# Optimization experiments

Measured on AMD Instinct MI355X. Metric: run time of the kernel, lower is better.

The kernel has to match this reference:

```python
import jax, jax.numpy as jnp
import numpy as np

B = 16
N = [20000, 5000, 1250, 313, 79]          # node counts per pooling level (fine -> coarse)
E = [120000, 30000, 7500, 1878, 474]      # ~6 edges per node (triangle mesh)
FILTERS = [3, 32, 32, 64, 64, 64]
K = 6
Z = 64
COND = 2
N_LAYERS = 4


def setup_inputs():
    ks = iter(jax.random.split(jax.random.key(0), 64))
    inp = {}
    inp["x"] = jax.random.normal(next(ks), (B * N[0], FILTERS[0]), jnp.float32)
    inp["label"] = jax.random.normal(next(ks), (B, COND), jnp.float32)
    for i in range(5):
        inp[f"edges{i}"] = jax.random.randint(next(ks), (2, E[i]), 0, N[i])
    for i in range(4):
        inp[f"ds_idx{i}"] = jax.random.randint(next(ks), (N[i + 1],), 0, N[i])
        inp[f"us_idx{i}"] = jax.random.randint(next(ks), (N[i], 3), 0, N[i + 1])
        inp[f"us_w{i}"] = jax.random.uniform(next(ks), (N[i], 3), jnp.float32)
    for i in range(4):
        inp[f"enc_w{i}"] = 0.1 * jax.random.normal(next(ks), (K, FILTERS[i], FILTERS[i + 1]), jnp.float32)
        inp[f"enc_b{i}"] = 0.1 * jax.random.normal(next(ks), (FILTERS[i + 1],), jnp.float32)
    for i in range(5):
        inp[f"dec_w{i}"] = 0.1 * jax.random.normal(next(ks), (K, FILTERS[-i - 1], FILTERS[-i - 2]), jnp.float32)
    for i in range(4):
        inp[f"dec_b{i}"] = 0.1 * jax.random.normal(next(ks), (FILTERS[-i - 2],), jnp.float32)
    lat_in = N[4] * FILTERS[-1]
    inp["enc_mu_w"] = 0.1 * jax.random.normal(next(ks), (lat_in, Z), jnp.float32)
    inp["enc_mu_b"] = jnp.zeros((Z,), jnp.float32)
    inp["enc_lv_w"] = 0.1 * jax.random.normal(next(ks), (lat_in, Z), jnp.float32)
    inp["enc_lv_b"] = jnp.zeros((Z,), jnp.float32)
    inp["dec_lin_w"] = 0.1 * jax.random.normal(next(ks), (Z + COND, lat_in), jnp.float32)
    inp["dec_lin_b"] = jnp.zeros((lat_in,), jnp.float32)
    return inp


def _sym_norm(edges, n):
    # ChebConv_Coma.norm: norm = D^-1/2[row] * w * D^-1/2[col], unit weights
    row, col = edges[0], edges[1]
    deg = jnp.zeros((n,), jnp.float32).at[row].add(1.0)
    dinv = jnp.where(deg > 0, deg ** -0.5, 0.0)
    return dinv[row] * dinv[col]


def _cheb(x, edges, norm, W, b):
    # Chebyshev recursion: Tx_0=x, Tx_1=L~x, Tx_k=2 L~ Tx_{k-1} - Tx_{k-2}
    src, tgt = edges[0], edges[1]

    def prop(h):  # h: [B, Nn, F] -> scatter-sum of norm-weighted source features
        return jnp.zeros_like(h).at[:, tgt].add(h[:, src] * norm[None, :, None])

    Tx0 = x
    out = jnp.einsum('bnf,fg->bng', Tx0, W[0])
    Tx1 = prop(x)
    out = out + jnp.einsum('bnf,fg->bng', Tx1, W[1])
    for k in range(2, W.shape[0]):
        Tx2 = 2.0 * prop(Tx1) - Tx0
        out = out + jnp.einsum('bnf,fg->bng', Tx2, W[k])
        Tx0, Tx1 = Tx1, Tx2
    return out if b is None else out + b


def _forward(x, label, us_ws, enc_ws, enc_bs, dec_ws, dec_bs,
             enc_mu_w, enc_mu_b, enc_lv_w, enc_lv_b, dec_lin_w, dec_lin_b,
             edges, norms, ds_idx, us_idx):
    h = x.reshape(B, N[0], FILTERS[0])
    # encoder
    for i in range(N_LAYERS):
        h = jax.nn.relu(_cheb(h, edges[i], norms[i], enc_ws[i], enc_bs[i]))
        h = h[:, ds_idx[i]]  # binary downsample matrix == row gather
    h = h.reshape(B, N[4] * FILTERS[-1])
    mu = h @ enc_mu_w + enc_mu_b
    logvar = h @ enc_lv_w + enc_lv_b
    # reparameterize (fixed eps for determinism)
    eps = jax.random.normal(jax.random.key(42), mu.shape, mu.dtype)
    z = mu + eps * jnp.exp(0.5 * logvar)
    # decoder
    h = jnp.concatenate([z, label], axis=1)
    h = jax.nn.relu(h @ dec_lin_w + dec_lin_b).reshape(B, N[4], FILTERS[-1])
    for i in range(N_LAYERS):
        lvl = N_LAYERS - 1 - i
        # barycentric upsample: 3 nonzeros per output row
        h = jnp.einsum('rk,brkf->brf', us_ws[lvl], h[:, us_idx[lvl]])
        h = jax.nn.relu(_cheb(h, edges[lvl], norms[lvl], dec_ws[i], dec_bs[i]))
    # faithful quirk of the original: final conv uses A_edge_index[-1] (coarsest graph edges)
    h = _cheb(h, edges[-1], norms[-1], dec_ws[4], None)
    return h.reshape(-1, FILTERS[0]), mu, logvar


def reference(x, label,
              edges0, edges1, edges2, edges3, edges4,
              ds_idx0, ds_idx1, ds_idx2, ds_idx3,
              us_idx0, us_idx1, us_idx2, us_idx3,
              us_w0, us_w1, us_w2, us_w3,
              enc_w0, enc_w1, enc_w2, enc_w3,
              enc_b0, enc_b1, enc_b2, enc_b3,
              dec_w0, dec_w1, dec_w2, dec_w3, dec_w4,
              dec_b0, dec_b1, dec_b2, dec_b3,
              enc_mu_w, enc_mu_b, enc_lv_w, enc_lv_b, dec_lin_w, dec_lin_b):
    edges = [edges0, edges1, edges2, edges3, edges4]
    norms = [_sym_norm(edges[i], N[i]) for i in range(5)]
    return _forward(x, label,
                    [us_w0, us_w1, us_w2, us_w3],
                    [enc_w0, enc_w1, enc_w2, enc_w3],
                    [enc_b0, enc_b1, enc_b2, enc_b3],
                    [dec_w0, dec_w1, dec_w2, dec_w3, dec_w4],
                    [dec_b0, dec_b1, dec_b2, dec_b3],
                    enc_mu_w, enc_mu_b, enc_lv_w, enc_lv_b, dec_lin_w, dec_lin_b,
                    edges, norms,
                    [ds_idx0, ds_idx1, ds_idx2, ds_idx3],
                    [us_idx0, us_idx1, us_idx2, us_idx3])
```

## Files before the change

kernel.cpp:

```cpp
#include <hip/hip_runtime.h>
#include <cstdint>
#include <cstddef>

#define WG 256
#define NB 16


struct IP5 { const int* e[5]; };
struct Ptr3 { const float* p[3]; };
struct WComb { const float* w[8]; float* c[8]; };

static __device__ __forceinline__ void fma4(float4& a, float s, const float4& b) {
  a.x = fmaf(s, b.x, a.x); a.y = fmaf(s, b.y, a.y);
  a.z = fmaf(s, b.z, a.z); a.w = fmaf(s, b.w, a.w);
}


__global__ void k_zero_i(int* __restrict__ p, int n) {
  int i = blockIdx.x * WG + threadIdx.x;
  if (i < n) p[i] = 0;
}

__global__ void k_hist_all(IP5 ep, int* __restrict__ dsrc, int* __restrict__ dtgt) {
  int i = blockIdx.x * WG + threadIdx.x;
  if (i >= 159852) return;
  int l, eo, ee, no, co;
  if (i < 120000)      { l = 0; eo = 0;      ee = 120000; no = 0;     co = 0; }
  else if (i < 150000) { l = 1; eo = 120000; ee = 30000;  no = 20000; co = 20000; }
  else if (i < 157500) { l = 2; eo = 150000; ee = 7500;   no = 25000; co = 25000; }
  else if (i < 159378) { l = 3; eo = 157500; ee = 1878;   no = 26250; co = 26250; }
  else                 { l = 4; eo = 159378; ee = 474;    no = 26563; co = 26563; }
  int e = i - eo;
  const int* E = ep.e[l];
  atomicAdd(&dsrc[no + E[e]], 1);
  atomicAdd(&dtgt[co + E[ee + e]], 1);
}

__global__ void k_scan_all(const int* __restrict__ deg_all, int* __restrict__ rowptr_all,
                           int* __restrict__ cursor_all) {
  static const int Ns[5] = {20000, 5000, 1250, 313, 20000};
  static const int CO[5] = {0, 20000, 25000, 26250, 26563};
  static const int RO[5] = {0, 20001, 25002, 26253, 26567};
  __shared__ int s[WG];
  int l = blockIdx.x;
  int N = Ns[l];
  const int* deg = deg_all + CO[l];
  int* rowptr = rowptr_all + RO[l];
  int* cursor = cursor_all + CO[l];
  int t = threadIdx.x;
  int chunk = (N + WG - 1) / WG;
  int a = t * chunk;
  int b = min(N, a + chunk);
  int sum = 0;
  for (int i = a; i < b; i++) sum += deg[i];
  s[t] = sum;
  __syncthreads();
  for (int off = 1; off < WG; off <<= 1) {
    int v = (t >= off) ? s[t - off] : 0;
    __syncthreads();
    s[t] += v;
    __syncthreads();
  }
  int run = (t == 0) ? 0 : s[t - 1];
  for (int i = a; i < b; i++) {
    rowptr[i] = run;
    cursor[i] = run;
    run += deg[i];
  }
  if (t == 0) rowptr[N] = s[WG - 1];
}

__global__ void k_combine(WComb wc) {
  static const int M[8] = {96, 1024, 2048, 4096, 4096, 4096, 2048, 1024};
  static const int OFF[8] = {0, 96, 1120, 3168, 7264, 11360, 15456, 17504};
  int i = blockIdx.x * WG + threadIdx.x;
  if (i >= 18528) return;
  int l = 0;
  while (l < 7 && i >= OFF[l + 1]) l++;
  int e = i - OFF[l], m = M[l];
  const float* w = wc.w[l];
  float* c = wc.c[l];
  float w0 = w[e], w1 = w[m + e], w2 = w[2 * m + e];
  float w3 = w[3 * m + e], w4 = w[4 * m + e], w5 = w[5 * m + e];
  c[e]         = w0 - w2 + w4;
  c[m + e]     = w1 - 3.f * w3 + 5.f * w5;
  c[2 * m + e] = 2.f * w2 - 8.f * w4;
  c[3 * m + e] = 4.f * w3 - 20.f * w5;
  c[4 * m + e] = 8.f * w4;
  c[5 * m + e] = 16.f * w5;
}


static __device__ __forceinline__ float erfinv_f(float x) {
  float w = -log1pf(-x * x);
  float p;
  if (w < 5.0f) {
    w -= 2.5f;
    p = 2.81022636e-08f;
    p = fmaf(p, w, 3.43273939e-07f);
    p = fmaf(p, w, -3.5233877e-06f);
    p = fmaf(p, w, -4.39150654e-06f);
    p = fmaf(p, w, 0.00021858087f);
    p = fmaf(p, w, -0.00125372503f);
    p = fmaf(p, w, -0.00417768164f);
    p = fmaf(p, w, 0.246640727f);
    p = fmaf(p, w, 1.50140941f);
  } else {
    w = sqrtf(w) - 3.0f;
    p = -0.000200214257f;
    p = fmaf(p, w, 0.000100950558f);
    p = fmaf(p, w, 0.00134934322f);
    p = fmaf(p, w, -0.00367342844f);
    p = fmaf(p, w, 0.00573950773f);
    p = fmaf(p, w, -0.0076224613f);
    p = fmaf(p, w, 0.00943887047f);
    p = fmaf(p, w, 1.00167406f);
    p = fmaf(p, w, 2.83297682f);
  }
  return p * x;
}

static __device__ __forceinline__ float bits_to_normal(unsigned b) {
  float f = __uint_as_float((b >> 9) | 0x3f800000u) - 1.0f;
  const float lo = -0.99999994f;
  float u = f * (1.0f - lo) + lo;
  u = fmaxf(u, lo);
  return 1.41421356f * erfinv_f(u);
}

static __device__ __forceinline__ float eps_val(int i) {
  unsigned x0 = 0u, x1 = (unsigned)i;
  unsigned ks[3] = {0u, 42u, 0u ^ 42u ^ 0x1BD11BDAu};
  x0 += ks[0];
  x1 += ks[1];
  const int R[2][4] = {{13, 15, 26, 6}, {17, 29, 16, 24}};
#pragma unroll
  for (int it = 0; it < 5; it++) {
#pragma unroll
    for (int j = 0; j < 4; j++) {
      x0 += x1;
      int r = R[it & 1][j];
      x1 = (x1 << r) | (x1 >> (32 - r));
      x1 ^= x0;
    }
    x0 += ks[(it + 1) % 3];
    x1 += ks[(it + 2) % 3] + (unsigned)(it + 1);
  }
  return bits_to_normal(x0 ^ x1);
}

__global__ void k_fill_all(IP5 ep, const int* __restrict__ dsrc, int* __restrict__ cursor,
                           int* __restrict__ csrc, float* __restrict__ csw,
                           float* __restrict__ eps, const float* __restrict__ x,
                           float* __restrict__ sxl) {
  int blk = blockIdx.x;
  if (blk < 625) {
    int i = blk * WG + threadIdx.x;
    if (i >= 159852) return;
    int l, eo, ee, no, co, eb;
    if (i < 120000)      { l = 0; eo = 0;      ee = 120000; no = 0;     co = 0;     eb = 0; }
    else if (i < 150000) { l = 1; eo = 120000; ee = 30000;  no = 20000; co = 20000; eb = 120000; }
    else if (i < 157500) { l = 2; eo = 150000; ee = 7500;   no = 25000; co = 25000; eb = 150000; }
    else if (i < 159378) { l = 3; eo = 157500; ee = 1878;   no = 26250; co = 26250; eb = 157500; }
    else                 { l = 4; eo = 159378; ee = 474;    no = 26563; co = 26563; eb = 159378; }
    int e = i - eo;
    const int* E = ep.e[l];
    int s = E[e], t = E[ee + e];
    float da = (float)dsrc[no + s], db = (float)dsrc[no + t];
    float wa = (da > 0.f) ? (1.0f / sqrtf(da)) : 0.f;
    float wb = (db > 0.f) ? (1.0f / sqrtf(db)) : 0.f;
    int pos = atomicAdd(&cursor[co + t], 1);
    csrc[eb + pos] = s;
    csw[eb + pos] = wa * wb;
  } else if (blk < 629) {
    int j = (blk - 625) * WG + threadIdx.x;
    if (j < 1024) eps[j] = eps_val(j);
  } else {
    int j = (blk - 629) * WG + threadIdx.x;
    if (j >= NB * 20000 * 3) return;
    int f = j % 3;
    int b = (j / 3) % NB;
    int n = j / 48;
    sxl[j] = x[((size_t)b * 20000 + n) * 3 + f];
  }
}


#define RFL_I(v) __builtin_amdgcn_readfirstlane(v)
#define RFL_F(v) __int_as_float(__builtin_amdgcn_readfirstlane(__float_as_int(v)))

template <int F>
__global__ __launch_bounds__(WG) void k_propw(const float* __restrict__ in,
                                              float* __restrict__ out,
                                              const int* __restrict__ rowptr,
                                              const int* __restrict__ csrc,
                                              const float* __restrict__ csw, int N) {
  constexpr int C4 = F / 16;
  int node = blockIdx.x * 4 + (threadIdx.x >> 6);
  if (node >= N) return;
  int lane = threadIdx.x & 63;
  const float4* in4 = (const float4*)in;
  float4 acc[C4];
#pragma unroll
  for (int u = 0; u < C4; u++) acc[u] = make_float4(0.f, 0.f, 0.f, 0.f);
  int beg = rowptr[node], end = rowptr[node + 1];
  int j = beg;
  for (; j + 3 < end; j += 4) {
    int s0 = RFL_I(csrc[j]);
    int s1 = RFL_I(csrc[j + 1]);
    int s2 = RFL_I(csrc[j + 2]);
    int s3 = RFL_I(csrc[j + 3]);
    float w0 = RFL_F(csw[j]);
    float w1 = RFL_F(csw[j + 1]);
    float w2 = RFL_F(csw[j + 2]);
    float w3 = RFL_F(csw[j + 3]);
    const float4* p0 = in4 + (size_t)s0 * (4 * F) + lane;
    const float4* p1 = in4 + (size_t)s1 * (4 * F) + lane;
    const float4* p2 = in4 + (size_t)s2 * (4 * F) + lane;
    const float4* p3 = in4 + (size_t)s3 * (4 * F) + lane;
    float4 v0[C4], v1[C4], v2[C4], v3[C4];
#pragma unroll
    for (int u = 0; u < C4; u++) v0[u] = p0[u * 64];
#pragma unroll
    for (int u = 0; u < C4; u++) v1[u] = p1[u * 64];
#pragma unroll
    for (int u = 0; u < C4; u++) v2[u] = p2[u * 64];
#pragma unroll
    for (int u = 0; u < C4; u++) v3[u] = p3[u * 64];
#pragma unroll
    for (int u = 0; u < C4; u++) {
      fma4(acc[u], w0, v0[u]);
      fma4(acc[u], w1, v1[u]);
      fma4(acc[u], w2, v2[u]);
      fma4(acc[u], w3, v3[u]);
    }
  }
  for (; j < end; j++) {
    int s0 = RFL_I(csrc[j]);
    float w0 = RFL_F(csw[j]);
    const float4* p0 = in4 + (size_t)s0 * (4 * F) + lane;
#pragma unroll
    for (int u = 0; u < C4; u++) {
      float4 v0 = p0[u * 64];
      fma4(acc[u], w0, v0);
    }
  }
  float4* o4 = (float4*)out + (size_t)node * (4 * F) + lane;
#pragma unroll
  for (int u = 0; u < C4; u++) o4[u * 64] = acc[u];
}

__global__ __launch_bounds__(WG) void k_propw3(const float* __restrict__ in,
                                               float* __restrict__ out,
                                               const int* __restrict__ rowptr,
                                               const int* __restrict__ csrc,
                                               const float* __restrict__ csw, int N) {
  int node = blockIdx.x * 4 + (threadIdx.x >> 6);
  if (node >= N) return;
  int lane = threadIdx.x & 63;
  if (lane >= 48) return;
  float acc = 0.f;
  int beg = rowptr[node], end = rowptr[node + 1];
  for (int j = beg; j < end; j++) {
    int s = RFL_I(csrc[j]);
    float w = RFL_F(csw[j]);
    acc = fmaf(w, in[(size_t)s * 48 + lane], acc);
  }
  out[(size_t)node * 48 + lane] = acc;
}


template <int F, int G>
__global__ __launch_bounds__(WG) void k_gemm3(Ptr3 txs, const float* __restrict__ W,
                                              const float* __restrict__ bias,
                                              float* __restrict__ out, int rows,
                                              const int* __restrict__ idx,
                                              int accum, int relu) {
  constexpr int CG = G / 4;
  constexpr int RT = WG / CG;
  constexpr int RPB = RT * 4;
  __shared__ float sW[3 * F * G];
  for (int i = threadIdx.x; i < 3 * F * G; i += WG) sW[i] = W[i];
  __syncthreads();
  int cg = threadIdx.x % CG;
  int rt = threadIdx.x / CG;
  int row0 = blockIdx.x * RPB + rt * 4;
  if (row0 >= rows) return;
  size_t src0 = row0;
  if (idx) {
    int node = row0 >> 4, b = row0 & 15;
    src0 = (size_t)idx[node] * 16 + b;
  }
  float* o = out + (size_t)row0 * G + cg * 4;
  float4 acc[4];
  if (accum) {
#pragma unroll
    for (int r = 0; r < 4; r++) acc[r] = *(const float4*)(o + (size_t)r * G);
  } else if (bias) {
    float4 bv = *(const float4*)(bias + cg * 4);
#pragma unroll
    for (int r = 0; r < 4; r++) acc[r] = bv;
  } else {
#pragma unroll
    for (int r = 0; r < 4; r++) acc[r] = make_float4(0.f, 0.f, 0.f, 0.f);
  }
#pragma unroll
  for (int kk = 0; kk < 3; kk++) {
    const float* tb = txs.p[kk] + src0 * F;
    const float* w = sW + kk * F * G + cg * 4;
    if constexpr (F == 3) {
      float4 w0 = *(const float4*)(w + 0 * G);
      float4 w1 = *(const float4*)(w + 1 * G);
      float4 w2 = *(const float4*)(w + 2 * G);
#pragma unroll
      for (int r = 0; r < 4; r++) {
        float x0 = tb[r * 3 + 0], x1 = tb[r * 3 + 1], x2 = tb[r * 3 + 2];
        fma4(acc[r], x0, w0);
        fma4(acc[r], x1, w1);
        fma4(acc[r], x2, w2);
      }
    } else {
#pragma unroll
      for (int fg = 0; fg < F / 4; fg++) {
        float4 xv[4];
#pragma unroll
        for (int r = 0; r < 4; r++) xv[r] = *(const float4*)(tb + (size_t)r * F + 4 * fg);
        float4 w0 = *(const float4*)(w + (4 * fg + 0) * G);
        float4 w1 = *(const float4*)(w + (4 * fg + 1) * G);
        float4 w2 = *(const float4*)(w + (4 * fg + 2) * G);
        float4 w3 = *(const float4*)(w + (4 * fg + 3) * G);
#pragma unroll
        for (int r = 0; r < 4; r++) {
          fma4(acc[r], xv[r].x, w0);
          fma4(acc[r], xv[r].y, w1);
          fma4(acc[r], xv[r].z, w2);
          fma4(acc[r], xv[r].w, w3);
        }
      }
    }
  }
  if (relu) {
#pragma unroll
    for (int r = 0; r < 4; r++) {
      acc[r].x = fmaxf(acc[r].x, 0.f); acc[r].y = fmaxf(acc[r].y, 0.f);
      acc[r].z = fmaxf(acc[r].z, 0.f); acc[r].w = fmaxf(acc[r].w, 0.f);
    }
  }
#pragma unroll
  for (int r = 0; r < 4; r++) *(float4*)(o + (size_t)r * G) = acc[r];
}

__global__ __launch_bounds__(WG) void k_gemm3_final(Ptr3 txs, const float* __restrict__ W,
                                                    const float* __restrict__ W4,
                                                    float* __restrict__ out,
                                                    float* __restrict__ dout, int rows) {
  constexpr int F = 32, G = 32;
  constexpr int CG = 8, RPB = 128;
  __shared__ float sW[3 * F * G];
  __shared__ float sWc[96];
  for (int i = threadIdx.x; i < 3 * F * G; i += WG) sW[i] = W[i];
  if (threadIdx.x < 96)
    sWc[threadIdx.x] = W4[threadIdx.x] - W4[192 + threadIdx.x] + W4[384 + threadIdx.x];
  __syncthreads();
  int cg = threadIdx.x % CG;
  int rt = threadIdx.x / CG;
  int row0 = blockIdx.x * RPB + rt * 4;
  float* o = out + (size_t)row0 * G + cg * 4;
  float4 acc[4];
#pragma unroll
  for (int r = 0; r < 4; r++) acc[r] = *(const float4*)(o + (size_t)r * G);
#pragma unroll
  for (int kk = 0; kk < 3; kk++) {
    const float* tb = txs.p[kk] + (size_t)row0 * F;
    const float* w = sW + kk * F * G + cg * 4;
#pragma unroll
    for (int fg = 0; fg < F / 4; fg++) {
      float4 xv[4];
#pragma unroll
      for (int r = 0; r < 4; r++) xv[r] = *(const float4*)(tb + (size_t)r * F + 4 * fg);
      float4 w0 = *(const float4*)(w + (4 * fg + 0) * G);
      float4 w1 = *(const float4*)(w + (4 * fg + 1) * G);
      float4 w2 = *(const float4*)(w + (4 * fg + 2) * G);
      float4 w3 = *(const float4*)(w + (4 * fg + 3) * G);
#pragma unroll
      for (int r = 0; r < 4; r++) {
        fma4(acc[r], xv[r].x, w0);
        fma4(acc[r], xv[r].y, w1);
        fma4(acc[r], xv[r].z, w2);
        fma4(acc[r], xv[r].w, w3);
      }
    }
  }
#pragma unroll
  for (int r = 0; r < 4; r++) {
    acc[r].x = fmaxf(acc[r].x, 0.f); acc[r].y = fmaxf(acc[r].y, 0.f);
    acc[r].z = fmaxf(acc[r].z, 0.f); acc[r].w = fmaxf(acc[r].w, 0.f);
  }
  if ((row0 >> 4) < 79) {
#pragma unroll
    for (int r = 0; r < 4; r++) *(float4*)(o + (size_t)r * G) = acc[r];
  }
#pragma unroll
  for (int r = 0; r < 4; r++) {
    float av[4] = {acc[r].x, acc[r].y, acc[r].z, acc[r].w};
    float p0 = 0.f, p1 = 0.f, p2 = 0.f;
#pragma unroll
    for (int j = 0; j < 4; j++) {
      int f = cg * 4 + j;
      p0 = fmaf(av[j], sWc[f * 3 + 0], p0);
      p1 = fmaf(av[j], sWc[f * 3 + 1], p1);
      p2 = fmaf(av[j], sWc[f * 3 + 2], p2);
    }
#pragma unroll
    for (int m = 4; m >= 1; m >>= 1) {
      p0 += __shfl_xor(p0, m, 64);
      p1 += __shfl_xor(p1, m, 64);
      p2 += __shfl_xor(p2, m, 64);
    }
    if (cg == 0) {
      int row = row0 + r;
      int n = row >> 4, b = row & 15;
      float* od = dout + ((size_t)b * 20000 + n) * 3;
      od[0] = p0; od[1] = p1; od[2] = p2;
    }
  }
}

__global__ __launch_bounds__(256) void k_final_fix(const float* __restrict__ in,
                                                   const float* __restrict__ W,
                                                   const int* __restrict__ rowptr,
                                                   const int* __restrict__ csrc,
                                                   const float* __restrict__ csw,
                                                   float* __restrict__ out) {
  __shared__ float B0[79 * 32], B1[79 * 32], B2[79 * 32];
  __shared__ float sacc[79 * 3];
  __shared__ float sW[576];
  int b = blockIdx.x, t = threadIdx.x;
  for (int i = t; i < 576; i += 256) sW[i] = W[i];
  for (int i = t; i < 2528; i += 256) {
    int r = i >> 5, f = i & 31;
    B0[i] = in[((size_t)r * 16 + b) * 32 + f];
  }
  __syncthreads();
  for (int i = t; i < 237; i += 256) {
    int r = i / 3, g = i % 3;
    float a = 0.f;
    for (int f = 0; f < 32; f++) a = fmaf(B0[r * 32 + f], sW[f * 3 + g], a);
    sacc[i] = a;
  }
  for (int i = t; i < 2528; i += 256) {
    int r = i >> 5, f = i & 31;
    float a = 0.f;
    for (int j = rowptr[r]; j < rowptr[r + 1]; j++) a = fmaf(csw[j], B0[csrc[j] * 32 + f], a);
    B1[i] = a;
  }
  __syncthreads();
  for (int i = t; i < 237; i += 256) {
    int r = i / 3, g = i % 3;
    float a = sacc[i];
    for (int f = 0; f < 32; f++) a = fmaf(B1[r * 32 + f], sW[96 + f * 3 + g], a);
    sacc[i] = a;
  }
  for (int i = t; i < 2528; i += 256) {
    int r = i >> 5, f = i & 31;
    float a = 0.f;
    for (int j = rowptr[r]; j < rowptr[r + 1]; j++) a = fmaf(csw[j], B1[csrc[j] * 32 + f], a);
    B2[i] = 2.f * a - B0[i];
  }
  __syncthreads();
  for (int i = t; i < 237; i += 256) {
    int r = i / 3, g = i % 3;
    float a = sacc[i];
    for (int f = 0; f < 32; f++) a = fmaf(B2[r * 32 + f], sW[192 + f * 3 + g], a);
    sacc[i] = a;
  }
  __syncthreads();
  for (int i = t; i < 2528; i += 256) {
    int r = i >> 5, f = i & 31;
    float a = 0.f;
    for (int j = rowptr[r]; j < rowptr[r + 1]; j++) a = fmaf(csw[j], B2[csrc[j] * 32 + f], a);
    B0[i] = 2.f * a - B1[i];
  }
  __syncthreads();
  for (int i = t; i < 237; i += 256) {
    int r = i / 3, g = i % 3;
    float a = sacc[i];
    for (int f = 0; f < 32; f++) a = fmaf(B0[r * 32 + f], sW[288 + f * 3 + g], a);
    sacc[i] = a;
  }
  __syncthreads();
  for (int i = t; i < 2528; i += 256) {
    int r = i >> 5, f = i & 31;
    float a = 0.f;
    for (int j = rowptr[r]; j < rowptr[r + 1]; j++) a = fmaf(csw[j], B0[csrc[j] * 32 + f], a);
    B1[i] = 2.f * a - B2[i];
  }
  __syncthreads();
  for (int i = t; i < 237; i += 256) {
    int r = i / 3, g = i % 3;
    float a = sacc[i];
    for (int f = 0; f < 32; f++) a = fmaf(B1[r * 32 + f], sW[384 + f * 3 + g], a);
    sacc[i] = a;
  }
  __syncthreads();
  for (int i = t; i < 2528; i += 256) {
    int r = i >> 5, f = i & 31;
    float a = 0.f;
    for (int j = rowptr[r]; j < rowptr[r + 1]; j++) a = fmaf(csw[j], B1[csrc[j] * 32 + f], a);
    B2[i] = 2.f * a - B0[i];
  }
  __syncthreads();
  for (int i = t; i < 237; i += 256) {
    int r = i / 3, g = i % 3;
    float a = sacc[i];
    for (int f = 0; f < 32; f++) a = fmaf(B2[r * 32 + f], sW[480 + f * 3 + g], a);
    out[((size_t)b * 20000 + r) * 3 + g] = a;
  }
}

template <int F>
__global__ __launch_bounds__(WG) void k_us(const float* __restrict__ in,
                                           float* __restrict__ out,
                                           const int* __restrict__ uidx,
                                           const float* __restrict__ uw, int Nf) {
  int i = blockIdx.x * WG + threadIdx.x;
  int total = Nf * NB * F;
  if (i >= total) return;
  int pos = i % (NB * F);
  int r = i / (NB * F);
  float acc = 0.f;
#pragma unroll
  for (int k = 0; k < 3; k++) {
    float v = in[(size_t)uidx[r * 3 + k] * NB * F + pos];
    acc = fmaf(uw[r * 3 + k], fmaxf(v, 0.f), acc);
  }
  out[i] = acc;
}


__global__ __launch_bounds__(64) void k_latent(const float* __restrict__ h,
                                               const float* __restrict__ muW,
                                               const float* __restrict__ muB,
                                               const float* __restrict__ lvW,
                                               const float* __restrict__ lvB,
                                               const float* __restrict__ eps,
                                               const float* __restrict__ label,
                                               float* __restrict__ mu_out,
                                               float* __restrict__ lv_out,
                                               float* __restrict__ hcat) {
  int b = blockIdx.x / 64;
  int g = blockIdx.x % 64;
  int l = threadIdx.x;
  float am = 0.f, al = 0.f;
  for (int i = l; i < 5056; i += 64) {
    int n = i >> 6, f = i & 63;
    float hv = h[(size_t)(n * 16 + b) * 64 + f];
    am = fmaf(hv, muW[(size_t)i * 64 + g], am);
    al = fmaf(hv, lvW[(size_t)i * 64 + g], al);
  }
  for (int off = 32; off > 0; off >>= 1) {
    am += __shfl_down(am, off, 64);
    al += __shfl_down(al, off, 64);
  }
  if (l == 0) {
    am += muB[g];
    al += lvB[g];
    mu_out[b * 64 + g] = am;
    lv_out[b * 64 + g] = al;
    hcat[b * 66 + g] = fmaf(eps[b * 64 + g], expf(0.5f * al), am);
    if (g < 2) hcat[b * 66 + 64 + g] = label[b * 2 + g];
  }
}

__global__ __launch_bounds__(WG) void k_declin(const float* __restrict__ hcat,
                                               const float* __restrict__ W,
                                               const float* __restrict__ bias,
                                               float* __restrict__ out) {
  int idx = blockIdx.x * WG + threadIdx.x;
  if (idx >= NB * 5056) return;
  int b = idx / 5056, j = idx % 5056;
  int n = j >> 6, f = j & 63;
  float acc = bias[j];
  const float* hc = hcat + b * 66;
#pragma unroll
  for (int i = 0; i < 66; i++) acc = fmaf(hc[i], W[(size_t)i * 5056 + j], acc);
  out[(size_t)(n * 16 + b) * 64 + f] = fmaxf(acc, 0.f);
}


static inline dim3 grid1(long n) { return dim3((unsigned)((n + WG - 1) / WG)); }

template <int F, int G>
static void run_cheb(float* in, float* out, float* A, float* B,
                     const float* C, const float* bias, int N, int Nout,
                     const int* ds_idx, int relu_last,
                     const int* rowptr, const int* csrc, const float* csw,
                     hipStream_t st) {
  int orows = NB * Nout;
  dim3 gP((unsigned)((N + 3) / 4));
  constexpr int RPB = (WG / (G / 4)) * 4;
  dim3 gG((unsigned)((orows + RPB - 1) / RPB));
  int relu2 = ds_idx ? 1 : relu_last;
  if constexpr (F == 3) {
    k_propw3<<<gP, WG, 0, st>>>(in, A, rowptr, csrc, csw, N);
    k_propw3<<<gP, WG, 0, st>>>(A, B, rowptr, csrc, csw, N);
    Ptr3 p1{{in, A, B}};
    k_gemm3<F, G><<<gG, WG, 0, st>>>(p1, C, bias, out, orows, ds_idx, 0, 0);
    k_propw3<<<gP, WG, 0, st>>>(B, in, rowptr, csrc, csw, N);
    k_propw3<<<gP, WG, 0, st>>>(in, A, rowptr, csrc, csw, N);
    k_propw3<<<gP, WG, 0, st>>>(A, B, rowptr, csrc, csw, N);
    Ptr3 p2{{in, A, B}};
    k_gemm3<F, G><<<gG, WG, 0, st>>>(p2, C + 3 * F * G, nullptr, out, orows, ds_idx, 1, relu2);
  } else {
    k_propw<F><<<gP, WG, 0, st>>>(in, A, rowptr, csrc, csw, N);
    k_propw<F><<<gP, WG, 0, st>>>(A, B, rowptr, csrc, csw, N);
    Ptr3 p1{{in, A, B}};
    k_gemm3<F, G><<<gG, WG, 0, st>>>(p1, C, bias, out, orows, ds_idx, 0, 0);
    k_propw<F><<<gP, WG, 0, st>>>(B, in, rowptr, csrc, csw, N);
    k_propw<F><<<gP, WG, 0, st>>>(in, A, rowptr, csrc, csw, N);
    k_propw<F><<<gP, WG, 0, st>>>(A, B, rowptr, csrc, csw, N);
    Ptr3 p2{{in, A, B}};
    k_gemm3<F, G><<<gG, WG, 0, st>>>(p2, C + 3 * F * G, nullptr, out, orows, ds_idx, 1, relu2);
  }
}

extern "C" void kernel_launch(void* const* d_in, const int* in_sizes, int n_in,
                              void* d_out, int out_size, void* d_ws, size_t ws_size,
                              hipStream_t stream) {
  const float* x = (const float*)d_in[0];
  const float* label = (const float*)d_in[1];
  IP5 ep;
  for (int l = 0; l < 5; l++) ep.e[l] = (const int*)d_in[2 + l];
  const int* ds_idx[4];
  const int* us_idx[4];
  const float* us_w[4];
  for (int i = 0; i < 4; i++) {
    ds_idx[i] = (const int*)d_in[7 + 3 * i];
    us_idx[i] = (const int*)d_in[8 + 3 * i];
    us_w[i] = (const float*)d_in[9 + 3 * i];
  }
  const float* enc_w[4];
  const float* enc_b[4];
  for (int i = 0; i < 4; i++) {
    enc_w[i] = (const float*)d_in[19 + 2 * i];
    enc_b[i] = (const float*)d_in[20 + 2 * i];
  }
  const float* dec_w[5];
  for (int i = 0; i < 5; i++) dec_w[i] = (const float*)d_in[27 + i];
  const float* dec_b[4];
  for (int i = 0; i < 4; i++) dec_b[i] = (const float*)d_in[32 + i];
  const float* mu_w = (const float*)d_in[36];
  const float* mu_b = (const float*)d_in[37];
  const float* lv_w = (const float*)d_in[38];
  const float* lv_b = (const float*)d_in[39];
  const float* dl_w = (const float*)d_in[40];
  const float* dl_b = (const float*)d_in[41];

  float* wsf = (float*)d_ws;
  size_t off = 0;
  auto carve = [&](size_t n) -> float* {
    float* p = wsf + off;
    off += (n + 63) & ~(size_t)63;
    return p;
  };
  const size_t SLOT = 10240000;
  float* s0 = carve(SLOT);
  float* s1 = carve(SLOT);
  float* s2 = carve(SLOT);
  float* s3 = carve(SLOT);
  float* sxl = carve(960000);
  int* deg_all = (int*)carve(26642 + 46563);
  int* deg_src_all = deg_all;
  int* deg_tgt_all = deg_all + 26642;
  int* rowptr_all = (int*)carve(46568);
  int* cursor_all = (int*)carve(46563);
  int* csrc_all = (int*)carve(159852);
  float* csw_all = carve(159852);
  float* eps = carve(1024);
  float* hcat = carve(1056);
  static const int CM[8] = {96, 1024, 2048, 4096, 4096, 4096, 2048, 1024};
  float* comb[8];
  for (int l = 0; l < 8; l++) comb[l] = carve((size_t)6 * CM[l]);

  static const int ROFF[5] = {0, 20001, 25002, 26253, 26567};
  static const int EOFF[5] = {0, 120000, 150000, 157500, 159378};
  auto RP = [&](int l) { return rowptr_all + ROFF[l]; };
  auto CS = [&](int l) { return csrc_all + EOFF[l]; };
  auto CW = [&](int l) { return csw_all + EOFF[l]; };

  k_zero_i<<<grid1(26642 + 46563), WG, 0, stream>>>(deg_all, 26642 + 46563);
  k_hist_all<<<grid1(159852), WG, 0, stream>>>(ep, deg_src_all, deg_tgt_all);
  k_scan_all<<<5, WG, 0, stream>>>(deg_tgt_all, rowptr_all, cursor_all);
  k_fill_all<<<625 + 4 + 3750, WG, 0, stream>>>(ep, deg_src_all, cursor_all, csrc_all,
                                                csw_all, eps, x, sxl);
  {
    WComb wc;
    for (int l = 0; l < 4; l++) { wc.w[l] = enc_w[l]; wc.c[l] = comb[l]; }
    for (int l = 0; l < 4; l++) { wc.w[4 + l] = dec_w[l]; wc.c[4 + l] = comb[4 + l]; }
    k_combine<<<grid1(18528), WG, 0, stream>>>(wc);
  }

  float* mu_out = (float*)d_out + 960000;
  float* lv_out = (float*)d_out + 961024;

  run_cheb<3, 32>(sxl, s1, s2, s3, comb[0], enc_b[0], 20000, 5000, ds_idx[0], 0,
                  RP(0), CS(0), CW(0), stream);
  run_cheb<32, 32>(s1, s0, s2, s3, comb[1], enc_b[1], 5000, 1250, ds_idx[1], 0,
                   RP(1), CS(1), CW(1), stream);
  run_cheb<32, 64>(s0, s1, s2, s3, comb[2], enc_b[2], 1250, 313, ds_idx[2], 0,
                   RP(2), CS(2), CW(2), stream);
  run_cheb<64, 64>(s1, s0, s2, s3, comb[3], enc_b[3], 313, 79, ds_idx[3], 0,
                   RP(3), CS(3), CW(3), stream);

  k_latent<<<1024, 64, 0, stream>>>(s0, mu_w, mu_b, lv_w, lv_b, eps, label, mu_out, lv_out, hcat);
  k_declin<<<grid1(NB * 5056), WG, 0, stream>>>(hcat, dl_w, dl_b, s0);

  k_us<64><<<grid1((long)313 * NB * 64), WG, 0, stream>>>(s0, s1, us_idx[3], us_w[3], 313);
  run_cheb<64, 64>(s1, s0, s2, s3, comb[4], dec_b[0], 313, 313, nullptr, 0,
                   RP(3), CS(3), CW(3), stream);
  k_us<64><<<grid1((long)1250 * NB * 64), WG, 0, stream>>>(s0, s1, us_idx[2], us_w[2], 1250);
  run_cheb<64, 64>(s1, s0, s2, s3, comb[5], dec_b[1], 1250, 1250, nullptr, 0,
                   RP(2), CS(2), CW(2), stream);
  k_us<64><<<grid1((long)5000 * NB * 64), WG, 0, stream>>>(s0, s1, us_idx[1], us_w[1], 5000);
  run_cheb<64, 32>(s1, s0, s2, s3, comb[6], dec_b[2], 5000, 5000, nullptr, 0,
                   RP(1), CS(1), CW(1), stream);
  k_us<32><<<grid1((long)20000 * NB * 32), WG, 0, stream>>>(s0, s1, us_idx[0], us_w[0], 20000);

  {
    const int N = 20000;
    int rows = NB * N;
    dim3 gP((unsigned)((N + 3) / 4));
    dim3 gG((unsigned)(rows / 128));
    k_propw<32><<<gP, WG, 0, stream>>>(s1, s2, RP(0), CS(0), CW(0), N);
    k_propw<32><<<gP, WG, 0, stream>>>(s2, s3, RP(0), CS(0), CW(0), N);
    Ptr3 p1{{s1, s2, s3}};
    k_gemm3<32, 32><<<gG, WG, 0, stream>>>(p1, comb[7], dec_b[3], s0, rows, nullptr, 0, 0);
    k_propw<32><<<gP, WG, 0, stream>>>(s3, s1, RP(0), CS(0), CW(0), N);
    k_propw<32><<<gP, WG, 0, stream>>>(s1, s2, RP(0), CS(0), CW(0), N);
    k_propw<32><<<gP, WG, 0, stream>>>(s2, s3, RP(0), CS(0), CW(0), N);
    Ptr3 p2{{s1, s2, s3}};
    k_gemm3_final<<<gG, WG, 0, stream>>>(p2, comb[7] + 3 * 32 * 32, dec_w[4], s0,
                                         (float*)d_out, rows);
  }

  k_final_fix<<<16, 256, 0, stream>>>(s0, dec_w[4], RP(4), CS(4), CW(4), (float*)d_out);
}
```

Measured before the change: 1.200 ms.

## Keep all Chebyshev terms live and fuse into one six-term GEMM per layer

```diff
diff --git a/kernel.cpp b/kernel.cpp
--- a/kernel.cpp
+++ b/kernel.cpp
@@ -8,6 +8,7 @@
 
 struct IP5 { const int* e[5]; };
 struct Ptr3 { const float* p[3]; };
+struct Ptr6 { const float* p[6]; };
 struct WComb { const float* w[8]; float* c[8]; };
 
 static __device__ __forceinline__ void fma4(float4& a, float s, const float4& b) {
@@ -350,21 +351,167 @@
   for (int r = 0; r < 4; r++) *(float4*)(o + (size_t)r * G) = acc[r];
 }
 
+
+template <int F>
+__global__ __launch_bounds__(WG) void k_gemm6(Ptr6 txs, const float* __restrict__ W,
+                                              const float* __restrict__ bias,
+                                              float* __restrict__ out, int rows,
+                                              const int* __restrict__ idx, int relu) {
+  constexpr int G = 32;
+  __shared__ float sW[6 * F * G];
+  for (int i = threadIdx.x; i < 6 * F * G; i += WG) sW[i] = W[i];
+  __syncthreads();
+  int cg = threadIdx.x & 7;
+  int rt = threadIdx.x >> 3;
+  int row0 = blockIdx.x * 128 + rt * 4;
+  if (row0 >= rows) return;
+  size_t src0 = row0;
+  if (idx) {
+    int node = row0 >> 4, b = row0 & 15;
+    src0 = (size_t)idx[node] * 16 + b;
+  }
+  float* o = out + (size_t)row0 * G + cg * 4;
+  float4 acc[4];
+  float4 bv = *(const float4*)(bias + cg * 4);
+#pragma unroll
+  for (int r = 0; r < 4; r++) acc[r] = bv;
+#pragma unroll
+  for (int kk = 0; kk < 6; kk++) {
+    const float* tb = txs.p[kk] + src0 * F;
+    const float* w = sW + kk * F * G + cg * 4;
+    if constexpr (F == 3) {
+      float4 w0 = *(const float4*)(w + 0 * G);
+      float4 w1 = *(const float4*)(w + 1 * G);
+      float4 w2 = *(const float4*)(w + 2 * G);
+#pragma unroll
+      for (int r = 0; r < 4; r++) {
+        float x0 = tb[r * 3 + 0], x1 = tb[r * 3 + 1], x2 = tb[r * 3 + 2];
+        fma4(acc[r], x0, w0);
+        fma4(acc[r], x1, w1);
+        fma4(acc[r], x2, w2);
+      }
+    } else {
+#pragma unroll
+      for (int fg = 0; fg < F / 4; fg++) {
+        float4 xv[4];
+#pragma unroll
+        for (int r = 0; r < 4; r++) xv[r] = *(const float4*)(tb + (size_t)r * F + 4 * fg);
+        float4 w0 = *(const float4*)(w + (4 * fg + 0) * G);
+        float4 w1 = *(const float4*)(w + (4 * fg + 1) * G);
+        float4 w2 = *(const float4*)(w + (4 * fg + 2) * G);
+        float4 w3 = *(const float4*)(w + (4 * fg + 3) * G);
+#pragma unroll
+        for (int r = 0; r < 4; r++) {
+          fma4(acc[r], xv[r].x, w0);
+          fma4(acc[r], xv[r].y, w1);
+          fma4(acc[r], xv[r].z, w2);
+          fma4(acc[r], xv[r].w, w3);
+        }
+      }
+    }
+  }
+  if (relu) {
+#pragma unroll
+    for (int r = 0; r < 4; r++) {
+      acc[r].x = fmaxf(acc[r].x, 0.f); acc[r].y = fmaxf(acc[r].y, 0.f);
+      acc[r].z = fmaxf(acc[r].z, 0.f); acc[r].w = fmaxf(acc[r].w, 0.f);
+    }
+  }
+#pragma unroll
+  for (int r = 0; r < 4; r++) *(float4*)(o + (size_t)r * G) = acc[r];
+}
+
+__global__ __launch_bounds__(WG) void k_gemm6f(Ptr6 txs, const float* __restrict__ W,
+                                               const float* __restrict__ bias,
+                                               const float* __restrict__ W4,
+                                               float* __restrict__ fixbuf,
+                                               float* __restrict__ dout, int rows) {
+  constexpr int F = 32, G = 32;
+  __shared__ float sW[6 * F * G];
+  __shared__ float sWc[96];
+  for (int i = threadIdx.x; i < 6 * F * G; i += WG) sW[i] = W[i];
+  if (threadIdx.x < 96)
+    sWc[threadIdx.x] = W4[threadIdx.x] - W4[192 + threadIdx.x] + W4[384 + threadIdx.x];
+  __syncthreads();
+  int cg = threadIdx.x & 7;
+  int rt = threadIdx.x >> 3;
+  int row0 = blockIdx.x * 128 + rt * 4;
+  float4 acc[4];
+  float4 bv = *(const float4*)(bias + cg * 4);
+#pragma unroll
+  for (int r = 0; r < 4; r++) acc[r] = bv;
+#pragma unroll
+  for (int kk = 0; kk < 6; kk++) {
+    const float* tb = txs.p[kk] + (size_t)row0 * F;
+    const float* w = sW + kk * F * G + cg * 4;
+#pragma unroll
+    for (int fg = 0; fg < F / 4; fg++) {
+      float4 xv[4];
+#pragma unroll
+      for (int r = 0; r < 4; r++) xv[r] = *(const float4*)(tb + (size_t)r * F + 4 * fg);
+      float4 w0 = *(const float4*)(w + (4 * fg + 0) * G);
+      float4 w1 = *(const float4*)(w + (4 * fg + 1) * G);
+      float4 w2 = *(const float4*)(w + (4 * fg + 2) * G);
+      float4 w3 = *(const float4*)(w + (4 * fg + 3) * G);
+#pragma unroll
+      for (int r = 0; r < 4; r++) {
+        fma4(acc[r], xv[r].x, w0);
+        fma4(acc[r], xv[r].y, w1);
+        fma4(acc[r], xv[r].z, w2);
+        fma4(acc[r], xv[r].w, w3);
+      }
+    }
+  }
+#pragma unroll
+  for (int r = 0; r < 4; r++) {
+    acc[r].x = fmaxf(acc[r].x, 0.f); acc[r].y = fmaxf(acc[r].y, 0.f);
+    acc[r].z = fmaxf(acc[r].z, 0.f); acc[r].w = fmaxf(acc[r].w, 0.f);
+  }
+  if ((row0 >> 4) < 79) {
+#pragma unroll
+    for (int r = 0; r < 4; r++)
+      *(float4*)(fixbuf + (size_t)(row0 + r) * 32 + cg * 4) = acc[r];
+  }
+#pragma unroll
+  for (int r = 0; r < 4; r++) {
+    float av[4] = {acc[r].x, acc[r].y, acc[r].z, acc[r].w};
+    float p0 = 0.f, p1 = 0.f, p2 = 0.f;
+#pragma unroll
+    for (int j = 0; j < 4; j++) {
+      int f = cg * 4 + j;
+      p0 = fmaf(av[j], sWc[f * 3 + 0], p0);
+      p1 = fmaf(av[j], sWc[f * 3 + 1], p1);
+      p2 = fmaf(av[j], sWc[f * 3 + 2], p2);
+    }
+#pragma unroll
+    for (int m = 4; m >= 1; m >>= 1) {
+      p0 += __shfl_xor(p0, m, 64);
+      p1 += __shfl_xor(p1, m, 64);
+      p2 += __shfl_xor(p2, m, 64);
+    }
+    if (cg == 0) {
+      int row = row0 + r;
+      int n = row >> 4, b = row & 15;
+      float* od = dout + ((size_t)b * 20000 + n) * 3;
+      od[0] = p0; od[1] = p1; od[2] = p2;
+    }
+  }
+}
+
 __global__ __launch_bounds__(WG) void k_gemm3_final(Ptr3 txs, const float* __restrict__ W,
                                                     const float* __restrict__ W4,
                                                     float* __restrict__ out,
                                                     float* __restrict__ dout, int rows) {
   constexpr int F = 32, G = 32;
-  constexpr int CG = 8, RPB = 128;
   __shared__ float sW[3 * F * G];
   __shared__ float sWc[96];
   for (int i = threadIdx.x; i < 3 * F * G; i += WG) sW[i] = W[i];
   if (threadIdx.x < 96)
     sWc[threadIdx.x] = W4[threadIdx.x] - W4[192 + threadIdx.x] + W4[384 + threadIdx.x];
   __syncthreads();
-  int cg = threadIdx.x % CG;
-  int rt = threadIdx.x / CG;
-  int row0 = blockIdx.x * RPB + rt * 4;
+  int cg = threadIdx.x & 7;
+  int rt = threadIdx.x >> 3;
+  int row0 = blockIdx.x * 128 + rt * 4;
   float* o = out + (size_t)row0 * G + cg * 4;
   float4 acc[4];
 #pragma unroll
@@ -624,6 +771,32 @@
   }
 }
 
+template <int F>
+static void run_cheb6(float* in, float* out, float* const* Y,
+                      const float* C, const float* bias, int N, int Nout,
+                      const int* ds_idx, int relu,
+                      const int* rowptr, const int* csrc, const float* csw,
+                      hipStream_t st) {
+  int orows = NB * Nout;
+  dim3 gP((unsigned)((N + 3) / 4));
+  dim3 gG((unsigned)((orows + 127) / 128));
+  if constexpr (F == 3) {
+    k_propw3<<<gP, WG, 0, st>>>(in, Y[0], rowptr, csrc, csw, N);
+    k_propw3<<<gP, WG, 0, st>>>(Y[0], Y[1], rowptr, csrc, csw, N);
+    k_propw3<<<gP, WG, 0, st>>>(Y[1], Y[2], rowptr, csrc, csw, N);
+    k_propw3<<<gP, WG, 0, st>>>(Y[2], Y[3], rowptr, csrc, csw, N);
+    k_propw3<<<gP, WG, 0, st>>>(Y[3], Y[4], rowptr, csrc, csw, N);
+  } else {
+    k_propw<F><<<gP, WG, 0, st>>>(in, Y[0], rowptr, csrc, csw, N);
+    k_propw<F><<<gP, WG, 0, st>>>(Y[0], Y[1], rowptr, csrc, csw, N);
+    k_propw<F><<<gP, WG, 0, st>>>(Y[1], Y[2], rowptr, csrc, csw, N);
+    k_propw<F><<<gP, WG, 0, st>>>(Y[2], Y[3], rowptr, csrc, csw, N);
+    k_propw<F><<<gP, WG, 0, st>>>(Y[3], Y[4], rowptr, csrc, csw, N);
+  }
+  Ptr6 p{{in, Y[0], Y[1], Y[2], Y[3], Y[4]}};
+  k_gemm6<F><<<gG, WG, 0, st>>>(p, C, bias, out, orows, ds_idx, relu);
+}
+
 extern "C" void kernel_launch(void* const* d_in, const int* in_sizes, int n_in,
                               void* d_out, int out_size, void* d_ws, size_t ws_size,
                               hipStream_t stream) {
@@ -678,9 +851,13 @@
   float* csw_all = carve(159852);
   float* eps = carve(1024);
   float* hcat = carve(1056);
+  float* fixbuf = carve(79 * 16 * 32);
   static const int CM[8] = {96, 1024, 2048, 4096, 4096, 4096, 2048, 1024};
   float* comb[8];
   for (int l = 0; l < 8; l++) comb[l] = carve((size_t)6 * CM[l]);
+  float* s4 = carve(SLOT);
+  float* s5 = carve(SLOT);
+  bool fused = (off * sizeof(float)) <= ws_size;
 
   static const int ROFF[5] = {0, 20001, 25002, 26253, 26567};
   static const int EOFF[5] = {0, 120000, 150000, 157500, 159378};
@@ -703,45 +880,77 @@
   float* mu_out = (float*)d_out + 960000;
   float* lv_out = (float*)d_out + 961024;
 
-  run_cheb<3, 32>(sxl, s1, s2, s3, comb[0], enc_b[0], 20000, 5000, ds_idx[0], 0,
-                  RP(0), CS(0), CW(0), stream);
-  run_cheb<32, 32>(s1, s0, s2, s3, comb[1], enc_b[1], 5000, 1250, ds_idx[1], 0,
-                   RP(1), CS(1), CW(1), stream);
-  run_cheb<32, 64>(s0, s1, s2, s3, comb[2], enc_b[2], 1250, 313, ds_idx[2], 0,
-                   RP(2), CS(2), CW(2), stream);
-  run_cheb<64, 64>(s1, s0, s2, s3, comb[3], enc_b[3], 313, 79, ds_idx[3], 0,
-                   RP(3), CS(3), CW(3), stream);
-
-  k_latent<<<1024, 64, 0, stream>>>(s0, mu_w, mu_b, lv_w, lv_b, eps, label, mu_out, lv_out, hcat);
-  k_declin<<<grid1(NB * 5056), WG, 0, stream>>>(hcat, dl_w, dl_b, s0);
-
-  k_us<64><<<grid1((long)313 * NB * 64), WG, 0, stream>>>(s0, s1, us_idx[3], us_w[3], 313);
-  run_cheb<64, 64>(s1, s0, s2, s3, comb[4], dec_b[0], 313, 313, nullptr, 0,
-                   RP(3), CS(3), CW(3), stream);
-  k_us<64><<<grid1((long)1250 * NB * 64), WG, 0, stream>>>(s0, s1, us_idx[2], us_w[2], 1250);
-  run_cheb<64, 64>(s1, s0, s2, s3, comb[5], dec_b[1], 1250, 1250, nullptr, 0,
-                   RP(2), CS(2), CW(2), stream);
-  k_us<64><<<grid1((long)5000 * NB * 64), WG, 0, stream>>>(s0, s1, us_idx[1], us_w[1], 5000);
-  run_cheb<64, 32>(s1, s0, s2, s3, comb[6], dec_b[2], 5000, 5000, nullptr, 0,
-                   RP(1), CS(1), CW(1), stream);
-  k_us<32><<<grid1((long)20000 * NB * 32), WG, 0, stream>>>(s0, s1, us_idx[0], us_w[0], 20000);
-
-  {
-    const int N = 20000;
-    int rows = NB * N;
-    dim3 gP((unsigned)((N + 3) / 4));
-    dim3 gG((unsigned)(rows / 128));
-    k_propw<32><<<gP, WG, 0, stream>>>(s1, s2, RP(0), CS(0), CW(0), N);
-    k_propw<32><<<gP, WG, 0, stream>>>(s2, s3, RP(0), CS(0), CW(0), N);
-    Ptr3 p1{{s1, s2, s3}};
-    k_gemm3<32, 32><<<gG, WG, 0, stream>>>(p1, comb[7], dec_b[3], s0, rows, nullptr, 0, 0);
-    k_propw<32><<<gP, WG, 0, stream>>>(s3, s1, RP(0), CS(0), CW(0), N);
-    k_propw<32><<<gP, WG, 0, stream>>>(s1, s2, RP(0), CS(0), CW(0), N);
-    k_propw<32><<<gP, WG, 0, stream>>>(s2, s3, RP(0), CS(0), CW(0), N);
-    Ptr3 p2{{s1, s2, s3}};
-    k_gemm3_final<<<gG, WG, 0, stream>>>(p2, comb[7] + 3 * 32 * 32, dec_w[4], s0,
-                                         (float*)d_out, rows);
-  }
-
-  k_final_fix<<<16, 256, 0, stream>>>(s0, dec_w[4], RP(4), CS(4), CW(4), (float*)d_out);
-}
+  if (fused) {
+    float* Ya[5] = {s1, s2, s3, s4, s5};
+    run_cheb6<3>(sxl, s0, Ya, comb[0], enc_b[0], 20000, 5000, ds_idx[0], 1,
+                 RP(0), CS(0), CW(0), stream);
+    run_cheb6<32>(s0, sxl, Ya, comb[1], enc_b[1], 5000, 1250, ds_idx[1], 1,
+                  RP(1), CS(1), CW(1), stream);
+    run_cheb<32, 64>(sxl, s0, s1, s2, comb[2], enc_b[2], 1250, 313, ds_idx[2], 0,
+                     RP(2), CS(2), CW(2), stream);
+    run_cheb<64, 64>(s0, s1, s2, s3, comb[3], enc_b[3], 313, 79, ds_idx[3], 0,
+                     RP(3), CS(3), CW(3), stream);
+    k_latent<<<1024, 64, 0, stream>>>(s1, mu_w, mu_b, lv_w, lv_b, eps, label, mu_out, lv_out, hcat);
+    k_declin<<<grid1(NB * 5056), WG, 0, stream>>>(hcat, dl_w, dl_b, s0);
+    k_us<64><<<grid1((long)313 * NB * 64), WG, 0, stream>>>(s0, s1, us_idx[3], us_w[3], 313);
+    run_cheb<64, 64>(s1, s0, s2, s3, comb[4], dec_b[0], 313, 313, nullptr, 0,
+                     RP(3), CS(3), CW(3), stream);
+    k_us<64><<<grid1((long)1250 * NB * 64), WG, 0, stream>>>(s0, s1, us_idx[2], us_w[2], 1250);
+    run_cheb<64, 64>(s1, s0, s2, s3, comb[5], dec_b[1], 1250, 1250, nullptr, 0,
+                     RP(2), CS(2), CW(2), stream);
+    k_us<64><<<grid1((long)5000 * NB * 64), WG, 0, stream>>>(s0, s1, us_idx[1], us_w[1], 5000);
+    run_cheb<64, 32>(s1, s0, s2, s3, comb[6], dec_b[2], 5000, 5000, nullptr, 0,
+                     RP(1), CS(1), CW(1), stream);
+    k_us<32><<<grid1((long)20000 * NB * 32), WG, 0, stream>>>(s0, s1, us_idx[0], us_w[0], 20000);
+    {
+      dim3 gP((unsigned)((20000 + 3) / 4));
+      k_propw<32><<<gP, WG, 0, stream>>>(s1, s2, RP(0), CS(0), CW(0), 20000);
+      k_propw<32><<<gP, WG, 0, stream>>>(s2, s3, RP(0), CS(0), CW(0), 20000);
+      k_propw<32><<<gP, WG, 0, stream>>>(s3, s4, RP(0), CS(0), CW(0), 20000);
+      k_propw<32><<<gP, WG, 0, stream>>>(s4, s5, RP(0), CS(0), CW(0), 20000);
+      k_propw<32><<<gP, WG, 0, stream>>>(s5, s0, RP(0), CS(0), CW(0), 20000);
+      Ptr6 p{{s1, s2, s3, s4, s5, s0}};
+      k_gemm6f<<<320000 / 128, WG, 0, stream>>>(p, comb[7], dec_b[3], dec_w[4],
+                                                fixbuf, (float*)d_out, 320000);
+    }
+  } else {
+    run_cheb<3, 32>(sxl, s1, s2, s3, comb[0], enc_b[0], 20000, 5000, ds_idx[0], 0,
+                    RP(0), CS(0), CW(0), stream);
+    run_cheb<32, 32>(s1, s0, s2, s3, comb[1], enc_b[1], 5000, 1250, ds_idx[1], 0,
+                     RP(1), CS(1), CW(1), stream);
+    run_cheb<32, 64>(s0, s1, s2, s3, comb[2], enc_b[2], 1250, 313, ds_idx[2], 0,
+                     RP(2), CS(2), CW(2), stream);
+    run_cheb<64, 64>(s1, s0, s2, s3, comb[3], enc_b[3], 313, 79, ds_idx[3], 0,
+                     RP(3), CS(3), CW(3), stream);
+    k_latent<<<1024, 64, 0, stream>>>(s0, mu_w, mu_b, lv_w, lv_b, eps, label, mu_out, lv_out, hcat);
+    k_declin<<<grid1(NB * 5056), WG, 0, stream>>>(hcat, dl_w, dl_b, s0);
+    k_us<64><<<grid1((long)313 * NB * 64), WG, 0, stream>>>(s0, s1, us_idx[3], us_w[3], 313);
+    run_cheb<64, 64>(s1, s0, s2, s3, comb[4], dec_b[0], 313, 313, nullptr, 0,
+                     RP(3), CS(3), CW(3), stream);
+    k_us<64><<<grid1((long)1250 * NB * 64), WG, 0, stream>>>(s0, s1, us_idx[2], us_w[2], 1250);
+    run_cheb<64, 64>(s1, s0, s2, s3, comb[5], dec_b[1], 1250, 1250, nullptr, 0,
+                     RP(2), CS(2), CW(2), stream);
+    k_us<64><<<grid1((long)5000 * NB * 64), WG, 0, stream>>>(s0, s1, us_idx[1], us_w[1], 5000);
+    run_cheb<64, 32>(s1, s0, s2, s3, comb[6], dec_b[2], 5000, 5000, nullptr, 0,
+                     RP(1), CS(1), CW(1), stream);
+    k_us<32><<<grid1((long)20000 * NB * 32), WG, 0, stream>>>(s0, s1, us_idx[0], us_w[0], 20000);
+    {
+      dim3 gP((unsigned)((20000 + 3) / 4));
+      dim3 gG((unsigned)(320000 / 128));
+      k_propw<32><<<gP, WG, 0, stream>>>(s1, s2, RP(0), CS(0), CW(0), 20000);
+      k_propw<32><<<gP, WG, 0, stream>>>(s2, s3, RP(0), CS(0), CW(0), 20000);
+      Ptr3 p1{{s1, s2, s3}};
+      k_gemm3<32, 32><<<gG, WG, 0, stream>>>(p1, comb[7], dec_b[3], s0, 320000, nullptr, 0, 0);
+      k_propw<32><<<gP, WG, 0, stream>>>(s3, s1, RP(0), CS(0), CW(0), 20000);
+      k_propw<32><<<gP, WG, 0, stream>>>(s1, s2, RP(0), CS(0), CW(0), 20000);
+      k_propw<32><<<gP, WG, 0, stream>>>(s2, s3, RP(0), CS(0), CW(0), 20000);
+      Ptr3 p2{{s1, s2, s3}};
+      k_gemm3_final<<<gG, WG, 0, stream>>>(p2, comb[7] + 3 * 32 * 32, dec_w[4], s0,
+                                           (float*)d_out, 320000);
+    }
+    k_final_fix<<<16, 256, 0, stream>>>(s0, dec_w[4], RP(4), CS(4), CW(4), (float*)d_out);
+    return;
+  }
+
+  k_final_fix<<<16, 256, 0, stream>>>(fixbuf, dec_w[4], RP(4), CS(4), CW(4), (float*)d_out);
+}
```

Measured after the change: 1.149 ms. 1.04x faster.
